# Kernel tuning notes

Measured on AMD Instinct MI355X. Metric: run time of the kernel, lower is better.

## Reference

```python
import jax, jax.numpy as jnp
import numpy as np

DIM = 1024
HEADS = 16
HEAD_DIM = DIM // HEADS


def setup_inputs() -> dict:
    key = jax.random.key(0)
    ks = jax.random.split(key, 5)
    x = jax.random.normal(ks[0], (4, 2048, DIM), dtype=jnp.float32)
    # torch Linear params: weight [out, in], bias [out]
    qkv_w = jax.random.normal(ks[1], (3 * DIM, DIM), dtype=jnp.float32) * (1.0 / np.sqrt(DIM))
    qkv_b = jax.random.normal(ks[2], (3 * DIM,), dtype=jnp.float32) * 0.01
    out_w = jax.random.normal(ks[3], (DIM, DIM), dtype=jnp.float32) * (1.0 / np.sqrt(DIM))
    out_b = jax.random.normal(ks[4], (DIM,), dtype=jnp.float32) * 0.01
    return {"x": x, "qkv_w": qkv_w, "qkv_b": qkv_b, "out_w": out_w, "out_b": out_b}


def reference(x, qkv_w, qkv_b, out_w, out_b):
    b, s, d = x.shape
    scale = 1.0 / np.sqrt(HEAD_DIM)
    qkv = x @ qkv_w.T + qkv_b                      # [b, s, 3d]
    qkv = qkv.reshape(b, s, 3, HEADS, HEAD_DIM)
    qkv = jnp.transpose(qkv, (2, 0, 3, 1, 4))      # [3, b, h, s, hd]
    q, k, v = qkv[0], qkv[1], qkv[2]
    attn = jnp.einsum('bhqd,bhkd->bhqk', q, k) * scale
    attn = jax.nn.softmax(attn, axis=-1)
    out = jnp.einsum('bhqk,bhkd->bhqd', attn, v)   # [b, h, s, hd]
    out = jnp.transpose(out, (0, 2, 1, 3)).reshape(b, s, d)
    return out @ out_w.T + out_b
```

## Files before the change

### kernel.cpp

```cpp
#include <hip/hip_runtime.h>

namespace {

constexpr int DIMC  = 1024;
constexpr int HEADS = 16;
constexpr int HD    = 64;
constexpr int BATCH = 4;
constexpr int SEQ   = 2048;
constexpr float SC2 = 0.18033688011112042f;

typedef __attribute__((ext_vector_type(8))) short short8;
typedef __attribute__((ext_vector_type(4))) float f32x4;

__device__ __forceinline__ unsigned short f2bf(float f) {
    union { float f; unsigned u; } v; v.f = f;
    unsigned r = v.u + 0x7fffu + ((v.u >> 16) & 1u);
    return (unsigned short)(r >> 16);
}

__device__ __forceinline__ float fexp2(float x) {
    float r;
    asm("v_exp_f32 %0, %1" : "=v"(r) : "v"(x));
    return r;
}

__device__ __forceinline__ void gl16(const unsigned short* gsrc, const unsigned short* ldst) {
    __builtin_amdgcn_global_load_lds(
        (const __attribute__((address_space(1))) void*)gsrc,
        (__attribute__((address_space(3))) void*)ldst, 16, 0, 0);
}

__global__ __launch_bounds__(256) void cvt3_f32_bf16(
    const float* __restrict__ x,  const float* __restrict__ wq,
    const float* __restrict__ wo,
    unsigned short* __restrict__ xb, unsigned short* __restrict__ wqb,
    unsigned short* __restrict__ wob)
{
    constexpr int N0 = 8192*1024/8;
    constexpr int N1 = 3072*1024/8;
    constexpr int N2 = 1024*1024/8;
    for (int i = blockIdx.x * blockDim.x + threadIdx.x; i < N0 + N1 + N2;
         i += gridDim.x * blockDim.x) {
        const float* src; unsigned short* dst; int j;
        if (i < N0)           { src = x;  dst = xb;  j = i; }
        else if (i < N0 + N1) { src = wq; dst = wqb; j = i - N0; }
        else                  { src = wo; dst = wob; j = i - N0 - N1; }
        const float4 a = ((const float4*)src)[2*j];
        const float4 b = ((const float4*)src)[2*j + 1];
        union { unsigned short s[8]; uint4 u; } p;
        p.s[0]=f2bf(a.x); p.s[1]=f2bf(a.y); p.s[2]=f2bf(a.z); p.s[3]=f2bf(a.w);
        p.s[4]=f2bf(b.x); p.s[5]=f2bf(b.y); p.s[6]=f2bf(b.z); p.s[7]=f2bf(b.w);
        ((uint4*)dst)[j] = p.u;
    }
}

template<int OUT_MODE>
__global__ __launch_bounds__(256) void gemm_bf16_mfma(
    const unsigned short* __restrict__ A, const unsigned short* __restrict__ W,
    const float* __restrict__ bias, void* __restrict__ Cout,
    unsigned short* __restrict__ vt,
    int M, int N, int K, int nbx)
{
    __shared__ __align__(16) char lds[32768];
    unsigned short* base = (unsigned short*)lds;

    const int tid = threadIdx.x;
    const int w = tid >> 6, l = tid & 63;
    const int wr = w >> 1, wc = w & 1;
    const int fr = l & 15, fq = l >> 4;

    const int qx  = gridDim.x >> 3;
    const int nid = (blockIdx.x & 7) * qx + (blockIdx.x >> 3);
    const int bx  = nid % nbx, by = nid / nbx;
    const int row0 = by * 128, col0 = bx * 128;

    const int sr0 = (w*2 + 0)*16 + (l >> 2);
    const int sr1 = (w*2 + 1)*16 + (l >> 2);
    const int skz = (((l & 3) ^ ((l >> 3) & 3))) * 8;

    const unsigned short* Ab0 = A + (size_t)(row0 + sr0)*K + skz;
    const unsigned short* Ab1 = A + (size_t)(row0 + sr1)*K + skz;
    const unsigned short* Wb0 = W + (size_t)(col0 + sr0)*K + skz;
    const unsigned short* Wb1 = W + (size_t)(col0 + sr1)*K + skz;

    f32x4 acc[4][4];
#pragma unroll
    for (int mi = 0; mi < 4; ++mi)
#pragma unroll
        for (int ni = 0; ni < 4; ++ni)
#pragma unroll
            for (int r = 0; r < 4; ++r) acc[mi][ni][r] = 0.f;

    const int cfa = (fq ^ ((fr >> 1) & 3)) * 8;

    auto stage = [&](int k0, int buf) {
        unsigned short* Ad = base + buf*8192;
        unsigned short* Wd = Ad + 4096;
        gl16(Ab0 + k0, Ad + (w*2 + 0)*512);
        gl16(Ab1 + k0, Ad + (w*2 + 1)*512);
        gl16(Wb0 + k0, Wd + (w*2 + 0)*512);
        gl16(Wb1 + k0, Wd + (w*2 + 1)*512);
    };

    stage(0, 0);
    for (int k0 = 0; k0 < K; k0 += 32) {
        const int buf = (k0 >> 5) & 1;
        __syncthreads();
        if (k0 + 32 < K) stage(k0 + 32, buf ^ 1);

        const unsigned short* Ac = base + buf*8192;
        const unsigned short* Wc = Ac + 4096;
        short8 af[4], bf[4];
#pragma unroll
        for (int mi = 0; mi < 4; ++mi)
            af[mi] = *(const short8*)(Ac + (wr*64 + mi*16 + fr)*32 + cfa);
#pragma unroll
        for (int ni = 0; ni < 4; ++ni)
            bf[ni] = *(const short8*)(Wc + (wc*64 + ni*16 + fr)*32 + cfa);
#pragma unroll
        for (int mi = 0; mi < 4; ++mi)
#pragma unroll
            for (int ni = 0; ni < 4; ++ni)
                acc[mi][ni] = __builtin_amdgcn_mfma_f32_16x16x32_bf16(
                    af[mi], bf[ni], acc[mi][ni], 0, 0, 0);
    }

    float bv[4];
#pragma unroll
    for (int ni = 0; ni < 4; ++ni) bv[ni] = bias[col0 + wc*64 + ni*16 + fr];
#pragma unroll
    for (int mi = 0; mi < 4; ++mi)
#pragma unroll
        for (int ni = 0; ni < 4; ++ni)
#pragma unroll
            for (int r = 0; r < 4; ++r) acc[mi][ni][r] += bv[ni];

    __syncthreads();
    float* rp = (float*)lds + w*1088;
    const int orow = l >> 2, oc = (l & 3) * 16;
    const bool vmode = (OUT_MODE == 2) && (col0 >= 2048);
    const int hh = vmode ? ((col0 + wc*64 - 2048) >> 6) : 0;

#pragma unroll
    for (int mi = 0; mi < 4; ++mi) {
#pragma unroll
        for (int ni = 0; ni < 4; ++ni)
#pragma unroll
            for (int r = 0; r < 4; ++r)
                rp[(fq*4 + r)*68 + ni*16 + fr] = acc[mi][ni][r];
        if (vmode) {
            float cv[16];
#pragma unroll
            for (int j = 0; j < 16; ++j) cv[j] = rp[j*68 + l];
            union { unsigned short s[16]; uint4 u[2]; } pk;
#pragma unroll
            for (int j = 0; j < 16; ++j) pk.s[j] = f2bf(cv[j]);
            const int srow0 = row0 + wr*64 + mi*16;
            const int bb = srow0 >> 11, ss = srow0 & 2047;
            unsigned short* dst = vt + ((size_t)((bb*16 + hh)*64 + l))*SEQ + ss;
            ((uint4*)dst)[0] = pk.u[0];
            ((uint4*)dst)[1] = pk.u[1];
        } else {
            float vrow[16];
#pragma unroll
            for (int j = 0; j < 4; ++j)
                *(f32x4*)&vrow[j*4] = *(const f32x4*)&rp[orow*68 + oc + j*4];
            const size_t grow = (size_t)(row0 + wr*64 + mi*16 + orow);
            const int    gcol = col0 + wc*64 + oc;
            if (OUT_MODE == 2) {
                union { unsigned short s[16]; uint4 u[2]; } pk;
#pragma unroll
                for (int j = 0; j < 16; ++j) pk.s[j] = f2bf(vrow[j]);
                uint4* dst = (uint4*)((unsigned short*)Cout + grow*N + gcol);
                dst[0] = pk.u[0]; dst[1] = pk.u[1];
            } else {
                float* dst = (float*)Cout + grow*N + gcol;
#pragma unroll
                for (int j = 0; j < 4; ++j)
                    *(f32x4*)(dst + j*4) = *(const f32x4*)&vrow[j*4];
            }
        }
    }
}

__global__ __launch_bounds__(256) void attn_mfma(
    const unsigned short* __restrict__ qkvb,
    const unsigned short* __restrict__ vt,
    unsigned short* __restrict__ ctxb)
{
    __shared__ __align__(16) char pool[51200];
    unsigned short* Kb0 = (unsigned short*)pool;
    unsigned short* Vb0 = Kb0 + 8192;
    unsigned short* Pl  = Kb0 + 16384;

    const int tid = threadIdx.x, w = tid >> 6, l = tid & 63;
    const int fr = l & 15, fq = l >> 4;

    const int bid = blockIdx.x;
    const int nid = (bid & 7) * 128 + (bid >> 3);
    const int b  = nid >> 8;
    const int h  = (nid >> 4) & 15;
    const int q0 = (nid & 15) * 128;
    const int wq = q0 + w*32;

    const unsigned short* qb = qkvb + (size_t)b*SEQ*3072 + h*64;
    const unsigned short* kb = qb + 1024;
    const unsigned short* vb = vt + (size_t)((b*16 + h)*64)*SEQ;

    auto scale8 = [](short8 v) -> short8 {
        union { short8 s; unsigned u[4]; } in, out;
        in.s = v;
#pragma unroll
        for (int i = 0; i < 4; ++i) {
            const float lo = __uint_as_float(in.u[i] << 16) * SC2;
            const float hi = __uint_as_float(in.u[i] & 0xffff0000u) * SC2;
            unsigned r;
            asm("v_cvt_pk_bf16_f32 %0, %1, %2" : "=v"(r) : "v"(lo), "v"(hi));
            out.u[i] = r;
        }
        return out.s;
    };
    short8 qf[2][2];
#pragma unroll
    for (int mf = 0; mf < 2; ++mf)
#pragma unroll
        for (int kk = 0; kk < 2; ++kk)
            qf[mf][kk] = scale8(*(const short8*)(qb + (size_t)(wq + mf*16 + fr)*3072
                                                 + kk*32 + fq*8));

    short8 ones;
#pragma unroll
    for (int i = 0; i < 8; ++i) ones[i] = (short)0x3F80;

    f32x4 z4;
#pragma unroll
    for (int r = 0; r < 4; ++r) z4[r] = 0.f;

    f32x4 o[2][4];
    f32x4 ol[2];
#pragma unroll
    for (int mf = 0; mf < 2; ++mf) {
#pragma unroll
        for (int df = 0; df < 4; ++df)
#pragma unroll
            for (int r = 0; r < 4; ++r) o[mf][df][r] = 0.f;
#pragma unroll
        for (int r = 0; r < 4; ++r) ol[mf][r] = 0.f;
    }

    const int srA = (w*2 + 0)*8 + (l >> 3);
    const int srB = (w*2 + 1)*8 + (l >> 3);
    const int scz = ((l & 7) ^ (l >> 3)) * 8;
    unsigned short* Pw = Pl + w*2304;

    const int c0e = (fq ^ (fr & 7)) * 8;
    const int c1e = c0e ^ 32;

    auto stage = [&](int kv0, int buf) {
        unsigned short* Kd = Kb0 + buf*4096;
        unsigned short* Vd = Vb0 + buf*4096;
        gl16(kb + (size_t)(kv0 + srA)*3072 + scz, Kd + (w*2 + 0)*512);
        gl16(kb + (size_t)(kv0 + srB)*3072 + scz, Kd + (w*2 + 1)*512);
        gl16(vb + (size_t)srA*SEQ + kv0 + scz,    Vd + (w*2 + 0)*512);
        gl16(vb + (size_t)srB*SEQ + kv0 + scz,    Vd + (w*2 + 1)*512);
    };

    stage(0, 0);
    for (int kv0 = 0; kv0 < SEQ; kv0 += 64) {
        const int buf = (kv0 >> 6) & 1;
        __syncthreads();
        if (kv0 + 64 < SEQ) stage(kv0 + 64, buf ^ 1);

        const unsigned short* Kc = Kb0 + buf*4096;
        const unsigned short* Vc = Vb0 + buf*4096;

        short8 vf[4][2];
#pragma unroll
        for (int df = 0; df < 4; ++df) {
            vf[df][0] = *(const short8*)(Vc + (df*16 + fr)*64 + c0e);
            vf[df][1] = *(const short8*)(Vc + (df*16 + fr)*64 + c1e);
        }

        f32x4 s[2][4];
#pragma unroll
        for (int nf = 0; nf < 4; ++nf) {
            const short8 k0f = *(const short8*)(Kc + (nf*16 + fr)*64 + c0e);
            const short8 k1f = *(const short8*)(Kc + (nf*16 + fr)*64 + c1e);
#pragma unroll
            for (int mf = 0; mf < 2; ++mf) {
                s[mf][nf] = __builtin_amdgcn_mfma_f32_16x16x32_bf16(k0f, qf[mf][0], z4, 0,0,0);
                s[mf][nf] = __builtin_amdgcn_mfma_f32_16x16x32_bf16(k1f, qf[mf][1], s[mf][nf], 0,0,0);
            }
        }

#pragma unroll
        for (int mf = 0; mf < 2; ++mf)
#pragma unroll
            for (int nf = 0; nf < 4; ++nf) {
                const float p0 = fexp2(s[mf][nf][0]);
                const float p1 = fexp2(s[mf][nf][1]);
                const float p2 = fexp2(s[mf][nf][2]);
                const float p3 = fexp2(s[mf][nf][3]);
                unsigned u0, u1;
                asm("v_cvt_pk_bf16_f32 %0, %1, %2" : "=v"(u0) : "v"(p0), "v"(p1));
                asm("v_cvt_pk_bf16_f32 %0, %1, %2" : "=v"(u1) : "v"(p2), "v"(p3));
                uint2 pw; pw.x = u0; pw.y = u1;
                *(uint2*)(Pw + (mf*16 + fr)*72 + nf*16 + fq*4) = pw;
            }

        short8 pa[2][2];
#pragma unroll
        for (int mf = 0; mf < 2; ++mf)
#pragma unroll
            for (int kk = 0; kk < 2; ++kk)
                pa[mf][kk] = *(const short8*)(Pw + (mf*16 + fr)*72 + kk*32 + fq*8);
#pragma unroll
        for (int mf = 0; mf < 2; ++mf) {
            ol[mf] = __builtin_amdgcn_mfma_f32_16x16x32_bf16(ones, pa[mf][0], ol[mf], 0,0,0);
            ol[mf] = __builtin_amdgcn_mfma_f32_16x16x32_bf16(ones, pa[mf][1], ol[mf], 0,0,0);
        }
#pragma unroll
        for (int df = 0; df < 4; ++df)
#pragma unroll
            for (int mf = 0; mf < 2; ++mf) {
                o[mf][df] = __builtin_amdgcn_mfma_f32_16x16x32_bf16(vf[df][0], pa[mf][0], o[mf][df], 0,0,0);
                o[mf][df] = __builtin_amdgcn_mfma_f32_16x16x32_bf16(vf[df][1], pa[mf][1], o[mf][df], 0,0,0);
            }
    }

    __syncthreads();
    float* rp = (float*)(pool + w*8704);
    const float inv0 = 1.f / ol[0][0], inv1 = 1.f / ol[1][0];
#pragma unroll
    for (int df = 0; df < 4; ++df) {
        f32x4 v0 = o[0][df] * inv0;
        f32x4 v1 = o[1][df] * inv1;
        *(f32x4*)&rp[(fr)*68      + df*16 + fq*4] = v0;
        *(f32x4*)&rp[(16 + fr)*68 + df*16 + fq*4] = v1;
    }
    const int orow = l >> 1, oc = (l & 1)*32;
    float vr[32];
#pragma unroll
    for (int j = 0; j < 8; ++j)
        *(f32x4*)&vr[j*4] = *(const f32x4*)&rp[orow*68 + oc + j*4];
    union { unsigned short s[32]; uint4 u[4]; } pk;
#pragma unroll
    for (int j = 0; j < 32; ++j) pk.s[j] = f2bf(vr[j]);
    unsigned short* dst = ctxb + (size_t)(b*SEQ + q0 + w*32 + orow)*DIMC + h*64 + oc;
#pragma unroll
    for (int j = 0; j < 4; ++j) *((uint4*)dst + j) = pk.u[j];
}

}

extern "C" void kernel_launch(void* const* d_in, const int* in_sizes, int n_in,
                              void* d_out, int out_size, void* d_ws, size_t ws_size,
                              hipStream_t stream)
{
    const float* x     = (const float*)d_in[0];
    const float* qkv_w = (const float*)d_in[1];
    const float* qkv_b = (const float*)d_in[2];
    const float* out_w = (const float*)d_in[3];
    const float* out_b = (const float*)d_in[4];

    unsigned short* xb   = (unsigned short*)d_ws;
    unsigned short* wqb  = xb   + (size_t)8192*1024;
    unsigned short* wob  = wqb  + (size_t)3072*1024;
    unsigned short* qkvb = wob  + (size_t)1024*1024;
    unsigned short* vtw  = qkvb + (size_t)8192*3072;
    unsigned short* ctxb = vtw  + (size_t)4096*2048;

    cvt3_f32_bf16<<<2048, 256, 0, stream>>>(x, qkv_w, out_w, xb, wqb, wob);

    gemm_bf16_mfma<2><<<dim3(1536), 256, 0, stream>>>(
        xb, wqb, qkv_b, (void*)qkvb, vtw, 8192, 3072, 1024, 24);

    attn_mfma<<<dim3(1024), 256, 0, stream>>>(qkvb, vtw, ctxb);

    gemm_bf16_mfma<0><<<dim3(512), 256, 0, stream>>>(
        ctxb, wob, out_b, d_out, nullptr, 8192, 1024, 1024, 8);
}
```

Baseline: 201.7 us.

## Double per-wave query rows in attention to reuse staged K/V tiles

Each wave in the attention kernel now processes 64 query rows (two 32-row halves) instead of 32. Each block therefore covers 256 queries and the grid is halved to 512 blocks. Every staged K/V tile and every V fragment read from LDS now feeds twice as many MFMAs, cutting shared-memory and global traffic per unit of work. The cost is more accumulator and Q registers per wave and fewer blocks to spread across the GPU.

```diff
diff --git a/kernel.cpp b/kernel.cpp
--- a/kernel.cpp
+++ b/kernel.cpp
@@ -197,11 +197,11 @@
     const int fr = l & 15, fq = l >> 4;
 
     const int bid = blockIdx.x;
-    const int nid = (bid & 7) * 128 + (bid >> 3);
-    const int b  = nid >> 8;
-    const int h  = (nid >> 4) & 15;
-    const int q0 = (nid & 15) * 128;
-    const int wq = q0 + w*32;
+    const int nid = (bid & 7) * 64 + (bid >> 3);
+    const int b  = nid >> 7;
+    const int h  = (nid >> 3) & 15;
+    const int q0 = (nid & 7) * 256;
+    const int wq = q0 + w*64;
 
     const unsigned short* qb = qkvb + (size_t)b*SEQ*3072 + h*64;
     const unsigned short* kb = qb + 1024;
@@ -220,9 +220,9 @@
         }
         return out.s;
     };
-    short8 qf[2][2];
-#pragma unroll
-    for (int mf = 0; mf < 2; ++mf)
+    short8 qf[4][2];
+#pragma unroll
+    for (int mf = 0; mf < 4; ++mf)
 #pragma unroll
         for (int kk = 0; kk < 2; ++kk)
             qf[mf][kk] = scale8(*(const short8*)(qb + (size_t)(wq + mf*16 + fr)*3072
@@ -236,10 +236,10 @@
 #pragma unroll
     for (int r = 0; r < 4; ++r) z4[r] = 0.f;
 
-    f32x4 o[2][4];
-    f32x4 ol[2];
-#pragma unroll
-    for (int mf = 0; mf < 2; ++mf) {
+    f32x4 o[4][4];
+    f32x4 ol[4];
+#pragma unroll
+    for (int mf = 0; mf < 4; ++mf) {
 #pragma unroll
         for (int df = 0; df < 4; ++df)
 #pragma unroll
@@ -281,74 +281,88 @@
             vf[df][1] = *(const short8*)(Vc + (df*16 + fr)*64 + c1e);
         }
 
-        f32x4 s[2][4];
-#pragma unroll
-        for (int nf = 0; nf < 4; ++nf) {
-            const short8 k0f = *(const short8*)(Kc + (nf*16 + fr)*64 + c0e);
-            const short8 k1f = *(const short8*)(Kc + (nf*16 + fr)*64 + c1e);
-#pragma unroll
-            for (int mf = 0; mf < 2; ++mf) {
-                s[mf][nf] = __builtin_amdgcn_mfma_f32_16x16x32_bf16(k0f, qf[mf][0], z4, 0,0,0);
-                s[mf][nf] = __builtin_amdgcn_mfma_f32_16x16x32_bf16(k1f, qf[mf][1], s[mf][nf], 0,0,0);
+#pragma unroll
+        for (int hf = 0; hf < 2; ++hf) {
+            f32x4 s[2][4];
+#pragma unroll
+            for (int nf = 0; nf < 4; ++nf) {
+                const short8 k0f = *(const short8*)(Kc + (nf*16 + fr)*64 + c0e);
+                const short8 k1f = *(const short8*)(Kc + (nf*16 + fr)*64 + c1e);
+#pragma unroll
+                for (int mfl = 0; mfl < 2; ++mfl) {
+                    s[mfl][nf] = __builtin_amdgcn_mfma_f32_16x16x32_bf16(
+                        k0f, qf[hf*2 + mfl][0], z4, 0,0,0);
+                    s[mfl][nf] = __builtin_amdgcn_mfma_f32_16x16x32_bf16(
+                        k1f, qf[hf*2 + mfl][1], s[mfl][nf], 0,0,0);
+                }
             }
-        }
-
-#pragma unroll
-        for (int mf = 0; mf < 2; ++mf)
-#pragma unroll
-            for (int nf = 0; nf < 4; ++nf) {
-                const float p0 = fexp2(s[mf][nf][0]);
-                const float p1 = fexp2(s[mf][nf][1]);
-                const float p2 = fexp2(s[mf][nf][2]);
-                const float p3 = fexp2(s[mf][nf][3]);
-                unsigned u0, u1;
-                asm("v_cvt_pk_bf16_f32 %0, %1, %2" : "=v"(u0) : "v"(p0), "v"(p1));
-                asm("v_cvt_pk_bf16_f32 %0, %1, %2" : "=v"(u1) : "v"(p2), "v"(p3));
-                uint2 pw; pw.x = u0; pw.y = u1;
-                *(uint2*)(Pw + (mf*16 + fr)*72 + nf*16 + fq*4) = pw;
+
+#pragma unroll
+            for (int mfl = 0; mfl < 2; ++mfl)
+#pragma unroll
+                for (int nf = 0; nf < 4; ++nf) {
+                    const float p0 = fexp2(s[mfl][nf][0]);
+                    const float p1 = fexp2(s[mfl][nf][1]);
+                    const float p2 = fexp2(s[mfl][nf][2]);
+                    const float p3 = fexp2(s[mfl][nf][3]);
+                    unsigned u0, u1;
+                    asm("v_cvt_pk_bf16_f32 %0, %1, %2" : "=v"(u0) : "v"(p0), "v"(p1));
+                    asm("v_cvt_pk_bf16_f32 %0, %1, %2" : "=v"(u1) : "v"(p2), "v"(p3));
+                    uint2 pw; pw.x = u0; pw.y = u1;
+                    *(uint2*)(Pw + (mfl*16 + fr)*72 + nf*16 + fq*4) = pw;
+                }
+
+            short8 pa[2][2];
+#pragma unroll
+            for (int mfl = 0; mfl < 2; ++mfl)
+#pragma unroll
+                for (int kk = 0; kk < 2; ++kk)
+                    pa[mfl][kk] = *(const short8*)(Pw + (mfl*16 + fr)*72 + kk*32 + fq*8);
+#pragma unroll
+            for (int mfl = 0; mfl < 2; ++mfl) {
+                ol[hf*2 + mfl] = __builtin_amdgcn_mfma_f32_16x16x32_bf16(
+                    ones, pa[mfl][0], ol[hf*2 + mfl], 0,0,0);
+                ol[hf*2 + mfl] = __builtin_amdgcn_mfma_f32_16x16x32_bf16(
+                    ones, pa[mfl][1], ol[hf*2 + mfl], 0,0,0);
             }
-
-        short8 pa[2][2];
-#pragma unroll
-        for (int mf = 0; mf < 2; ++mf)
-#pragma unroll
-            for (int kk = 0; kk < 2; ++kk)
-                pa[mf][kk] = *(const short8*)(Pw + (mf*16 + fr)*72 + kk*32 + fq*8);
-#pragma unroll
-        for (int mf = 0; mf < 2; ++mf) {
-            ol[mf] = __builtin_amdgcn_mfma_f32_16x16x32_bf16(ones, pa[mf][0], ol[mf], 0,0,0);
-            ol[mf] = __builtin_amdgcn_mfma_f32_16x16x32_bf16(ones, pa[mf][1], ol[mf], 0,0,0);
-        }
-#pragma unroll
-        for (int df = 0; df < 4; ++df)
-#pragma unroll
-            for (int mf = 0; mf < 2; ++mf) {
-                o[mf][df] = __builtin_amdgcn_mfma_f32_16x16x32_bf16(vf[df][0], pa[mf][0], o[mf][df], 0,0,0);
-                o[mf][df] = __builtin_amdgcn_mfma_f32_16x16x32_bf16(vf[df][1], pa[mf][1], o[mf][df], 0,0,0);
-            }
+#pragma unroll
+            for (int df = 0; df < 4; ++df)
+#pragma unroll
+                for (int mfl = 0; mfl < 2; ++mfl) {
+                    o[hf*2 + mfl][df] = __builtin_amdgcn_mfma_f32_16x16x32_bf16(
+                        vf[df][0], pa[mfl][0], o[hf*2 + mfl][df], 0,0,0);
+                    o[hf*2 + mfl][df] = __builtin_amdgcn_mfma_f32_16x16x32_bf16(
+                        vf[df][1], pa[mfl][1], o[hf*2 + mfl][df], 0,0,0);
+                }
+        }
     }
 
     __syncthreads();
     float* rp = (float*)(pool + w*8704);
-    const float inv0 = 1.f / ol[0][0], inv1 = 1.f / ol[1][0];
-#pragma unroll
-    for (int df = 0; df < 4; ++df) {
-        f32x4 v0 = o[0][df] * inv0;
-        f32x4 v1 = o[1][df] * inv1;
-        *(f32x4*)&rp[(fr)*68      + df*16 + fq*4] = v0;
-        *(f32x4*)&rp[(16 + fr)*68 + df*16 + fq*4] = v1;
-    }
     const int orow = l >> 1, oc = (l & 1)*32;
-    float vr[32];
-#pragma unroll
-    for (int j = 0; j < 8; ++j)
-        *(f32x4*)&vr[j*4] = *(const f32x4*)&rp[orow*68 + oc + j*4];
-    union { unsigned short s[32]; uint4 u[4]; } pk;
-#pragma unroll
-    for (int j = 0; j < 32; ++j) pk.s[j] = f2bf(vr[j]);
-    unsigned short* dst = ctxb + (size_t)(b*SEQ + q0 + w*32 + orow)*DIMC + h*64 + oc;
-#pragma unroll
-    for (int j = 0; j < 4; ++j) *((uint4*)dst + j) = pk.u[j];
+#pragma unroll
+    for (int hf = 0; hf < 2; ++hf) {
+        const float inv0 = 1.f / ol[hf*2 + 0][0];
+        const float inv1 = 1.f / ol[hf*2 + 1][0];
+#pragma unroll
+        for (int df = 0; df < 4; ++df) {
+            f32x4 v0 = o[hf*2 + 0][df] * inv0;
+            f32x4 v1 = o[hf*2 + 1][df] * inv1;
+            *(f32x4*)&rp[(fr)*68      + df*16 + fq*4] = v0;
+            *(f32x4*)&rp[(16 + fr)*68 + df*16 + fq*4] = v1;
+        }
+        float vr[32];
+#pragma unroll
+        for (int j = 0; j < 8; ++j)
+            *(f32x4*)&vr[j*4] = *(const f32x4*)&rp[orow*68 + oc + j*4];
+        union { unsigned short s[32]; uint4 u[4]; } pk;
+#pragma unroll
+        for (int j = 0; j < 32; ++j) pk.s[j] = f2bf(vr[j]);
+        unsigned short* dst = ctxb
+            + (size_t)(b*SEQ + q0 + w*64 + hf*32 + orow)*DIMC + h*64 + oc;
+#pragma unroll
+        for (int j = 0; j < 4; ++j) *((uint4*)dst + j) = pk.u[j];
+    }
 }
 
 }
@@ -375,7 +389,7 @@
     gemm_bf16_mfma<2><<<dim3(1536), 256, 0, stream>>>(
         xb, wqb, qkv_b, (void*)qkvb, vtw, 8192, 3072, 1024, 24);
 
-    attn_mfma<<<dim3(1024), 256, 0, stream>>>(qkvb, vtw, ctxb);
+    attn_mfma<<<dim3(512), 256, 0, stream>>>(qkvb, vtw, ctxb);
 
     gemm_bf16_mfma<0><<<dim3(512), 256, 0, stream>>>(
         ctxb, wob, out_b, d_out, nullptr, 8192, 1024, 1024, 8);
```

Result: no change. 198.3 us (-1.7%).

## Halve attention KV tile to 32 keys to cut LDS and registers

Applied to the files above, without the earlier changes.

Shrinks the per-iteration key/value tile in the attention kernel from 64 to 32 keys. This halves the K/V double buffers and the P scratch, cutting shared memory per block from about 50KB to 34KB, and reduces the score and V fragment registers. V staging gets a new swizzle for its 32-wide rows. The intent is higher occupancy, at the cost of twice as many loop iterations and barriers, less work per sync, and shorter prefetch distance.

```diff
diff --git a/kernel.cpp b/kernel.cpp
--- a/kernel.cpp
+++ b/kernel.cpp
@@ -188,10 +188,8 @@
     const unsigned short* __restrict__ vt,
     unsigned short* __restrict__ ctxb)
 {
-    __shared__ __align__(16) char pool[51200];
-    unsigned short* Kb0 = (unsigned short*)pool;
-    unsigned short* Vb0 = Kb0 + 8192;
-    unsigned short* Pl  = Kb0 + 16384;
+    __shared__ __align__(16) char pool[34816];
+    unsigned short* hw = (unsigned short*)pool;
 
     const int tid = threadIdx.x, w = tid >> 6, l = tid & 63;
     const int fr = l & 15, fq = l >> 4;
@@ -248,44 +246,41 @@
         for (int r = 0; r < 4; ++r) ol[mf][r] = 0.f;
     }
 
-    const int srA = (w*2 + 0)*8 + (l >> 3);
-    const int srB = (w*2 + 1)*8 + (l >> 3);
-    const int scz = ((l & 7) ^ (l >> 3)) * 8;
-    unsigned short* Pw = Pl + w*2304;
-
-    const int c0e = (fq ^ (fr & 7)) * 8;
-    const int c1e = c0e ^ 32;
+    const int srK  = w*8 + (l >> 3);
+    const int sczK = ((l & 7) ^ (l >> 3)) * 8;
+    const int srV  = w*16 + (l >> 2);
+    const int sczV = ((l & 3) ^ ((w*8 + (l >> 3)) & 3)) * 8;
+
+    unsigned short* Pw = hw + 8192 + w*1280;
+
+    const int cK0 = (fq ^ (fr & 7)) * 8;
+    const int cK1 = cK0 ^ 32;
+    const int cV  = (fq ^ ((fr >> 1) & 3)) * 8;
 
     auto stage = [&](int kv0, int buf) {
-        unsigned short* Kd = Kb0 + buf*4096;
-        unsigned short* Vd = Vb0 + buf*4096;
-        gl16(kb + (size_t)(kv0 + srA)*3072 + scz, Kd + (w*2 + 0)*512);
-        gl16(kb + (size_t)(kv0 + srB)*3072 + scz, Kd + (w*2 + 1)*512);
-        gl16(vb + (size_t)srA*SEQ + kv0 + scz,    Vd + (w*2 + 0)*512);
-        gl16(vb + (size_t)srB*SEQ + kv0 + scz,    Vd + (w*2 + 1)*512);
+        gl16(kb + (size_t)(kv0 + srK)*3072 + sczK, hw + buf*2048 + w*512);
+        gl16(vb + (size_t)srV*SEQ + kv0 + sczV,    hw + 4096 + buf*2048 + w*512);
     };
 
     stage(0, 0);
-    for (int kv0 = 0; kv0 < SEQ; kv0 += 64) {
-        const int buf = (kv0 >> 6) & 1;
+    for (int kv0 = 0; kv0 < SEQ; kv0 += 32) {
+        const int buf = (kv0 >> 5) & 1;
         __syncthreads();
-        if (kv0 + 64 < SEQ) stage(kv0 + 64, buf ^ 1);
-
-        const unsigned short* Kc = Kb0 + buf*4096;
-        const unsigned short* Vc = Vb0 + buf*4096;
-
-        short8 vf[4][2];
-#pragma unroll
-        for (int df = 0; df < 4; ++df) {
-            vf[df][0] = *(const short8*)(Vc + (df*16 + fr)*64 + c0e);
-            vf[df][1] = *(const short8*)(Vc + (df*16 + fr)*64 + c1e);
-        }
-
-        f32x4 s[2][4];
-#pragma unroll
-        for (int nf = 0; nf < 4; ++nf) {
-            const short8 k0f = *(const short8*)(Kc + (nf*16 + fr)*64 + c0e);
-            const short8 k1f = *(const short8*)(Kc + (nf*16 + fr)*64 + c1e);
+        if (kv0 + 32 < SEQ) stage(kv0 + 32, buf ^ 1);
+
+        const unsigned short* Kc = hw + buf*2048;
+        const unsigned short* Vc = hw + 4096 + buf*2048;
+
+        short8 vf[4];
+#pragma unroll
+        for (int df = 0; df < 4; ++df)
+            vf[df] = *(const short8*)(Vc + (df*16 + fr)*32 + cV);
+
+        f32x4 s[2][2];
+#pragma unroll
+        for (int nf = 0; nf < 2; ++nf) {
+            const short8 k0f = *(const short8*)(Kc + (nf*16 + fr)*64 + cK0);
+            const short8 k1f = *(const short8*)(Kc + (nf*16 + fr)*64 + cK1);
 #pragma unroll
             for (int mf = 0; mf < 2; ++mf) {
                 s[mf][nf] = __builtin_amdgcn_mfma_f32_16x16x32_bf16(k0f, qf[mf][0], z4, 0,0,0);
@@ -296,7 +291,7 @@
 #pragma unroll
         for (int mf = 0; mf < 2; ++mf)
 #pragma unroll
-            for (int nf = 0; nf < 4; ++nf) {
+            for (int nf = 0; nf < 2; ++nf) {
                 const float p0 = fexp2(s[mf][nf][0]);
                 const float p1 = fexp2(s[mf][nf][1]);
                 const float p2 = fexp2(s[mf][nf][2]);
@@ -305,27 +300,22 @@
                 asm("v_cvt_pk_bf16_f32 %0, %1, %2" : "=v"(u0) : "v"(p0), "v"(p1));
                 asm("v_cvt_pk_bf16_f32 %0, %1, %2" : "=v"(u1) : "v"(p2), "v"(p3));
                 uint2 pw; pw.x = u0; pw.y = u1;
-                *(uint2*)(Pw + (mf*16 + fr)*72 + nf*16 + fq*4) = pw;
+                *(uint2*)(Pw + (mf*16 + fr)*40 + nf*16 + fq*4) = pw;
             }
 
-        short8 pa[2][2];
+        short8 pa[2];
 #pragma unroll
         for (int mf = 0; mf < 2; ++mf)
-#pragma unroll
-            for (int kk = 0; kk < 2; ++kk)
-                pa[mf][kk] = *(const short8*)(Pw + (mf*16 + fr)*72 + kk*32 + fq*8);
-#pragma unroll
-        for (int mf = 0; mf < 2; ++mf) {
-            ol[mf] = __builtin_amdgcn_mfma_f32_16x16x32_bf16(ones, pa[mf][0], ol[mf], 0,0,0);
-            ol[mf] = __builtin_amdgcn_mfma_f32_16x16x32_bf16(ones, pa[mf][1], ol[mf], 0,0,0);
-        }
+            pa[mf] = *(const short8*)(Pw + (mf*16 + fr)*40 + fq*8);
+#pragma unroll
+        for (int mf = 0; mf < 2; ++mf)
+            ol[mf] = __builtin_amdgcn_mfma_f32_16x16x32_bf16(ones, pa[mf], ol[mf], 0,0,0);
 #pragma unroll
         for (int df = 0; df < 4; ++df)
 #pragma unroll
-            for (int mf = 0; mf < 2; ++mf) {
-                o[mf][df] = __builtin_amdgcn_mfma_f32_16x16x32_bf16(vf[df][0], pa[mf][0], o[mf][df], 0,0,0);
-                o[mf][df] = __builtin_amdgcn_mfma_f32_16x16x32_bf16(vf[df][1], pa[mf][1], o[mf][df], 0,0,0);
-            }
+            for (int mf = 0; mf < 2; ++mf)
+                o[mf][df] = __builtin_amdgcn_mfma_f32_16x16x32_bf16(
+                    vf[df], pa[mf], o[mf][df], 0,0,0);
     }
 
     __syncthreads();
```

Measured after the change: 199.6 us. Within noise of the previous version (-1.0%).
